# Kernel tuning notes

Measured on AMD Instinct MI355X. Metric: run time of the kernel, lower is better.

Reference implementation:

```python
import jax, jax.numpy as jnp
import numpy as np

HEAD_NUM = 16

def setup_inputs() -> dict:
    key = jax.random.key(0)
    k1, k2, k3, k4, k5 = jax.random.split(key, 5)
    B, S, F = 4, 2048, 1024
    return {
        "X": jax.random.normal(k1, (B, S, F), dtype=jnp.float32),
        "residual_score": jax.random.normal(k2, (B, S, F), dtype=jnp.float32),
        "wq": jax.random.normal(k3, (F, F), dtype=jnp.float32) * 0.05,
        "wk": jax.random.normal(k4, (F, F), dtype=jnp.float32) * 0.05,
        "wv": jax.random.normal(k5, (F, F), dtype=jnp.float32) * 0.05,
    }

def reference(X, residual_score, wq, wk, wv):
    B, S, F = X.shape
    H = HEAD_NUM
    D = F // H  # head dim
    # Original scales logits by sqrt(seq_len / head_num), not sqrt(head_dim).
    scale = jnp.sqrt(jnp.asarray(S / H, dtype=X.dtype))
    # QKV projections: [B,S,F] @ [F,F] -> [B,S,F], then split features into heads -> [B,H,S,D]
    def proj(w):
        y = jnp.einsum('bsf,fg->bsg', X, w)
        return y.reshape(B, S, H, D).transpose(0, 2, 1, 3)
    q, k, v = proj(wq), proj(wk), proj(wv)
    logits = jnp.einsum('bhsd,bhtd->bhst', q, k) / scale  # [B,H,S,S]
    attn = jax.nn.softmax(logits, axis=-1)
    effect = jnp.einsum('bhst,bhtd->bhsd', attn, v)  # [B,H,S,D]
    all_effects = effect.transpose(0, 2, 1, 3).reshape(B, S, F)
    out = all_effects + residual_score
    return (out, out)
```

## Files before the change

### kernel.cpp

```cpp
#include <hip/hip_runtime.h>
#include <hip/hip_bf16.h>
#include <stdint.h>

#define B_ 4
#define S_ 2048
#define F_ 1024
#define H_ 16
#define D_ 64
#define M_ (B_*S_)
#define OUTHALF ((size_t)B_*S_*F_)
#define KVB 64
#define QBLK 256

typedef __attribute__((ext_vector_type(4))) float f32x4;
typedef __attribute__((ext_vector_type(8))) short bf16x8;

__device__ __forceinline__ short f2bf(float f) {
  __hip_bfloat16 h = __float2bfloat16(f);
  return *reinterpret_cast<short*>(&h);
}

__device__ __forceinline__ void gl2lds16(const short* g, short* l) {
  __builtin_amdgcn_global_load_lds(
      (const __attribute__((address_space(1))) uint32_t*)g,
      (__attribute__((address_space(3))) uint32_t*)l, 16, 0, 0);
}

#define VMCNT_BAR(N)                                            \
  do {                                                          \
    asm volatile("s_waitcnt vmcnt(" #N ")" ::: "memory");       \
    __builtin_amdgcn_s_barrier();                               \
    asm volatile("" ::: "memory");                              \
  } while (0)

__global__ __launch_bounds__(256) void prep(
    const float* __restrict__ X, short* __restrict__ Xb,
    const float* __restrict__ wq, const float* __restrict__ wk, const float* __restrict__ wv,
    short* __restrict__ tq, short* __restrict__ tk, short* __restrict__ tv) {
  __shared__ float tile[32][33];
  const int bid = blockIdx.x;
  const int tid = threadIdx.x;
  if (bid < (M_ * F_) / (256 * 8)) {
    int i = (bid * 256 + tid) * 8;
    f32x4 a = *(const f32x4*)(X + i);
    f32x4 b = *(const f32x4*)(X + i + 4);
    bf16x8 o;
    o[0]=f2bf(a[0]); o[1]=f2bf(a[1]); o[2]=f2bf(a[2]); o[3]=f2bf(a[3]);
    o[4]=f2bf(b[0]); o[5]=f2bf(b[1]); o[6]=f2bf(b[2]); o[7]=f2bf(b[3]);
    *(bf16x8*)(Xb + i) = o;
    return;
  }
  const int b2 = bid - (M_ * F_) / (256 * 8);
  const int z = b2 >> 10;
  const int rem = b2 & 1023;
  const int bx = rem & 31, by = rem >> 5;
  const float* W = z == 0 ? wq : (z == 1 ? wk : wv);
  short* T = z == 0 ? tq : (z == 1 ? tk : tv);
  const int tx = tid & 31, ty = tid >> 5;
  int x = bx * 32 + tx;
  int y0 = by * 32;
  #pragma unroll
  for (int j = ty; j < 32; j += 8) tile[j][tx] = W[(size_t)(y0 + j) * F_ + x];
  __syncthreads();
  int x2 = y0 + tx;
  int y2 = bx * 32;
  #pragma unroll
  for (int j = ty; j < 32; j += 8) T[(size_t)(y2 + j) * F_ + x2] = f2bf(tile[tx][j]);
}

__global__ __launch_bounds__(256) void gemm_qkv(
    const short* __restrict__ Xb,
    const short* __restrict__ Wtq, const short* __restrict__ Wtk, const short* __restrict__ Wtv,
    short* __restrict__ Qb, short* __restrict__ Kb, short* __restrict__ Vt) {
  __shared__ short SMEM[4][4096];
  const int z = blockIdx.z;
  const short* Wt = z == 0 ? Wtq : (z == 1 ? Wtk : Wtv);
  const int m0 = blockIdx.x * 128, n0 = blockIdx.y * 128;
  const int tid = threadIdx.x, wid = tid >> 6, lane = tid & 63;
  const int wm = wid >> 1, wn = wid & 1;
  const int l15 = lane & 15, l4 = lane >> 4;

  f32x4 acc[4][4];
  #pragma unroll
  for (int i = 0; i < 4; ++i)
    #pragma unroll
    for (int j = 0; j < 4; ++j) acc[i][j] = {0.f, 0.f, 0.f, 0.f};

  const int srow = wid * 32 + (lane >> 2);
  const int scol = ((lane & 3) ^ ((lane >> 3) & 3)) * 8;
  const int rchunk = ((l15 >> 1) & 3);

  auto stage = [&](int buf, int k0) {
    gl2lds16(Xb + (size_t)(m0 + srow) * F_ + k0 + scol,      &SMEM[buf][(wid * 32) * 32]);
    gl2lds16(Xb + (size_t)(m0 + srow + 16) * F_ + k0 + scol, &SMEM[buf][(wid * 32 + 16) * 32]);
    gl2lds16(Wt + (size_t)(n0 + srow) * F_ + k0 + scol,      &SMEM[2 + buf][(wid * 32) * 32]);
    gl2lds16(Wt + (size_t)(n0 + srow + 16) * F_ + k0 + scol, &SMEM[2 + buf][(wid * 32 + 16) * 32]);
  };

  stage(0, 0);
  const int NT = F_ / 32;
  for (int t = 0; t < NT; ++t) {
    const int buf = t & 1;
    if (t + 1 < NT) {
      stage(buf ^ 1, (t + 1) * 32);
      VMCNT_BAR(4);
    } else {
      VMCNT_BAR(0);
    }
    bf16x8 a[4], b[4];
    const int rc = (l4 ^ rchunk) * 8;
    #pragma unroll
    for (int mf = 0; mf < 4; ++mf)
      a[mf] = *(const bf16x8*)&SMEM[buf][(wm * 64 + mf * 16 + l15) * 32 + rc];
    #pragma unroll
    for (int nf = 0; nf < 4; ++nf)
      b[nf] = *(const bf16x8*)&SMEM[2 + buf][(wn * 64 + nf * 16 + l15) * 32 + rc];
    __builtin_amdgcn_s_setprio(1);
    #pragma unroll
    for (int mf = 0; mf < 4; ++mf)
      #pragma unroll
      for (int nf = 0; nf < 4; ++nf)
        acc[mf][nf] = __builtin_amdgcn_mfma_f32_16x16x32_bf16(a[mf], b[nf], acc[mf][nf], 0, 0, 0);
    __builtin_amdgcn_s_setprio(0);
    __builtin_amdgcn_s_barrier();
    asm volatile("" ::: "memory");
  }

  const float qscale = 0.12751784477559752f;

  if (z == 2) {
    #pragma unroll
    for (int mf = 0; mf < 4; ++mf)
      #pragma unroll
      for (int nf = 0; nf < 4; ++nf)
        #pragma unroll
        for (int r = 0; r < 4; ++r) {
          float v = acc[mf][nf][r];
          int row = m0 + wm * 64 + mf * 16 + l4 * 4 + r;
          int col = n0 + wn * 64 + nf * 16 + l15;
          int bb = row >> 11, s = row & 2047, h = col >> 6, d = col & 63;
          int s5 = s & 31;
          int sp = (s & ~31) | (((s5 >> 2) & 3) << 3) | (((s5 >> 4) & 1) << 2) | (s5 & 3);
          Vt[((size_t)(bb * H_ + h) * D_ + d) * S_ + sp] = f2bf(v);
        }
  } else {
    short* Ep = &SMEM[0][0];
    short* dstBase = (z == 0) ? Qb : Kb;
    const float qs = (z == 0) ? qscale : 1.f;
    #pragma unroll
    for (int p = 0; p < 2; ++p) {
      __syncthreads();
      if (wm == p) {
        #pragma unroll
        for (int mf = 0; mf < 4; ++mf)
          #pragma unroll
          for (int nf = 0; nf < 4; ++nf)
            #pragma unroll
            for (int r = 0; r < 4; ++r)
              Ep[(mf * 16 + l4 * 4 + r) * 136 + wn * 64 + nf * 16 + l15] =
                  f2bf(acc[mf][nf][r] * qs);
      }
      __syncthreads();
      const int rr = tid >> 2, qt = tid & 3;
      const int grow = m0 + p * 64 + rr;
      const int gcol = n0 + qt * 32;
      const int bb = grow >> 11, s = grow & 2047;
      const int h = gcol >> 6, d0 = gcol & 63;
      short* dst = dstBase + (((size_t)(bb * H_ + h) * S_ + s) * D_ + d0);
      #pragma unroll
      for (int k = 0; k < 4; ++k)
        *(bf16x8*)(dst + k * 8) = *(const bf16x8*)&Ep[rr * 136 + qt * 32 + k * 8];
    }
  }
}

__global__ __launch_bounds__(512, 4) void attn_kernel(
    const short* __restrict__ Qb, const short* __restrict__ Kb, const short* __restrict__ Vt,
    const float* __restrict__ resid, float* __restrict__ out) {
  __shared__ short Ks[2][KVB][64];
  __shared__ short Vs[2][D_][KVB];
  const int bh = blockIdx.x;
  const int b = bh >> 4, h = bh & 15;
  const int qbase = blockIdx.y * QBLK;
  const int wid = threadIdx.x >> 6, lane = threadIdx.x & 63;
  const int l15 = lane & 15, l4 = lane >> 4;
  const short* Qp = Qb + (size_t)bh * S_ * D_;
  const short* Kp = Kb + (size_t)bh * S_ * D_;
  const short* Vp = Vt + (size_t)bh * D_ * S_;

  bf16x8 bq[2][2];
  #pragma unroll
  for (int g = 0; g < 2; ++g) {
    int qr = qbase + wid * 32 + g * 16 + l15;
    bq[g][0] = *(const bf16x8*)&Qp[qr * D_ + l4 * 8];
    bq[g][1] = *(const bf16x8*)&Qp[qr * D_ + 32 + l4 * 8];
  }

  bf16x8 aOnes;
  {
    short onebf = (short)0x3F80;
    #pragma unroll
    for (int i = 0; i < 8; ++i) aOnes[i] = (l15 == 0) ? onebf : (short)0;
  }

  const int sr = wid * 8 + (lane >> 3);
  const int ssrc = ((lane & 7) ^ (lane >> 3)) * 8;

  f32x4 acc[2][4];
  f32x4 accl[2];
  #pragma unroll
  for (int g = 0; g < 2; ++g) {
    accl[g] = {0.f, 0.f, 0.f, 0.f};
    #pragma unroll
    for (int df = 0; df < 4; ++df) acc[g][df] = {0.f, 0.f, 0.f, 0.f};
  }

  gl2lds16(Kp + (0 + sr) * D_ + ssrc, &Ks[0][wid * 8][0]);
  gl2lds16(Vp + (size_t)sr * S_ + 0 + ssrc, &Vs[0][wid * 8][0]);

  const int NT = S_ / KVB;
  for (int t = 0; t < NT; ++t) {
    const int buf = t & 1;
    __syncthreads();
    if (t + 1 < NT) {
      const int kv1 = (t + 1) * KVB;
      gl2lds16(Kp + (kv1 + sr) * D_ + ssrc, &Ks[buf ^ 1][wid * 8][0]);
      gl2lds16(Vp + (size_t)sr * S_ + kv1 + ssrc, &Vs[buf ^ 1][wid * 8][0]);
    }

    f32x4 sf[2][4];
    #pragma unroll
    for (int g = 0; g < 2; ++g)
      #pragma unroll
      for (int nf = 0; nf < 4; ++nf) sf[g][nf] = {0.f, 0.f, 0.f, 0.f};
    __builtin_amdgcn_s_setprio(1);
    #pragma unroll
    for (int nf = 0; nf < 4; ++nf) {
      int row = nf * 16 + l15;
      int c0 = (l4 ^ (row & 7)) * 8;
      int c1 = ((4 + l4) ^ (row & 7)) * 8;
      bf16x8 ak0 = *(const bf16x8*)&Ks[buf][row][c0];
      bf16x8 ak1 = *(const bf16x8*)&Ks[buf][row][c1];
      #pragma unroll
      for (int g = 0; g < 2; ++g) {
        sf[g][nf] = __builtin_amdgcn_mfma_f32_16x16x32_bf16(ak0, bq[g][0], sf[g][nf], 0, 0, 0);
        sf[g][nf] = __builtin_amdgcn_mfma_f32_16x16x32_bf16(ak1, bq[g][1], sf[g][nf], 0, 0, 0);
      }
    }
    __builtin_amdgcn_s_setprio(0);

    __builtin_amdgcn_s_setprio(1);
    #pragma unroll
    for (int bb = 0; bb < 2; ++bb) {
      bf16x8 p0, p1;
      #pragma unroll
      for (int r = 0; r < 4; ++r) {
        p0[r]     = f2bf(__builtin_amdgcn_exp2f(sf[0][2 * bb][r]));
        p0[4 + r] = f2bf(__builtin_amdgcn_exp2f(sf[0][2 * bb + 1][r]));
        p1[r]     = f2bf(__builtin_amdgcn_exp2f(sf[1][2 * bb][r]));
        p1[4 + r] = f2bf(__builtin_amdgcn_exp2f(sf[1][2 * bb + 1][r]));
      }
      #pragma unroll
      for (int df = 0; df < 4; ++df) {
        int row = df * 16 + l15;
        bf16x8 av = *(const bf16x8*)&Vs[buf][row][((4 * bb + l4) ^ (row & 7)) * 8];
        acc[0][df] = __builtin_amdgcn_mfma_f32_16x16x32_bf16(av, p0, acc[0][df], 0, 0, 0);
        acc[1][df] = __builtin_amdgcn_mfma_f32_16x16x32_bf16(av, p1, acc[1][df], 0, 0, 0);
      }
      accl[0] = __builtin_amdgcn_mfma_f32_16x16x32_bf16(aOnes, p0, accl[0], 0, 0, 0);
      accl[1] = __builtin_amdgcn_mfma_f32_16x16x32_bf16(aOnes, p1, accl[1], 0, 0, 0);
    }
    __builtin_amdgcn_s_setprio(0);
  }

  #pragma unroll
  for (int g = 0; g < 2; ++g) {
    float lg = __shfl(accl[g][0], l15);
    float rl = 1.f / lg;
    int s = qbase + wid * 32 + g * 16 + l15;
    #pragma unroll
    for (int df = 0; df < 4; ++df) {
      size_t oi = ((size_t)b * S_ + s) * F_ + h * D_ + df * 16 + l4 * 4;
      f32x4 rv = *(const f32x4*)&resid[oi];
      f32x4 ov;
      #pragma unroll
      for (int r = 0; r < 4; ++r) ov[r] = acc[g][df][r] * rl + rv[r];
      *(f32x4*)&out[oi] = ov;
      *(f32x4*)&out[oi + OUTHALF] = ov;
    }
  }
}

extern "C" void kernel_launch(void* const* d_in, const int* in_sizes, int n_in,
                              void* d_out, int out_size, void* d_ws, size_t ws_size,
                              hipStream_t stream) {
  (void)in_sizes; (void)n_in; (void)out_size; (void)ws_size;
  const float* X     = (const float*)d_in[0];
  const float* resid = (const float*)d_in[1];
  const float* wq    = (const float*)d_in[2];
  const float* wk    = (const float*)d_in[3];
  const float* wv    = (const float*)d_in[4];
  float* out = (float*)d_out;
  char* ws = (char*)d_ws;
  short* Xb  = (short*)(ws);
  short* Wtq = (short*)(ws + (16u << 20));
  short* Wtk = (short*)(ws + (18u << 20));
  short* Wtv = (short*)(ws + (20u << 20));
  short* Qb  = (short*)(ws + (22u << 20));
  short* Kb  = (short*)(ws + (38u << 20));
  short* Vt  = (short*)(ws + (54u << 20));

  prep<<<dim3((M_ * F_) / (256 * 8) + 3 * 1024), 256, 0, stream>>>(
      X, Xb, wq, wk, wv, Wtq, Wtk, Wtv);
  gemm_qkv<<<dim3(M_ / 128, F_ / 128, 3), 256, 0, stream>>>(Xb, Wtq, Wtk, Wtv, Qb, Kb, Vt);
  attn_kernel<<<dim3(B_ * H_, S_ / QBLK), 512, 0, stream>>>(Qb, Kb, Vt, resid, out);
}
```

Baseline: 168.2 us.

## Double KV tile to 128 and interleave QK and PV per 32-key chunk

Raises the KV block to 128 keys, so there are half as many loop iterations and barriers. Each thread now issues two K and two V async loads per tile, and the V swizzle is widened to 16 chunks. Inside the loop, the full score tile is no longer computed before the exponentials. Each 32-key chunk now does its QK MFMAs, exp and PV MFMAs in turn, which lowers live score registers. The cost is double the LDS buffer size, which may reduce occupancy.

```diff
diff --git a/kernel.cpp b/kernel.cpp
--- a/kernel.cpp
+++ b/kernel.cpp
@@ -9,7 +9,7 @@
 #define D_ 64
 #define M_ (B_*S_)
 #define OUTHALF ((size_t)B_*S_*F_)
-#define KVB 64
+#define KVB 128
 #define QBLK 256
 
 typedef __attribute__((ext_vector_type(4))) float f32x4;
@@ -203,8 +203,10 @@
     for (int i = 0; i < 8; ++i) aOnes[i] = (l15 == 0) ? onebf : (short)0;
   }
 
-  const int sr = wid * 8 + (lane >> 3);
-  const int ssrc = ((lane & 7) ^ (lane >> 3)) * 8;
+  const int ksr = wid * 16 + (lane >> 3);
+  const int ksc = ((lane & 7) ^ (ksr & 7)) * 8;
+  const int vr = wid * 4 + (lane >> 4);
+  const int vsc = ((lane & 15) ^ (vr & 15)) * 8;
 
   f32x4 acc[2][4];
   f32x4 accl[2];
@@ -215,8 +217,10 @@
     for (int df = 0; df < 4; ++df) acc[g][df] = {0.f, 0.f, 0.f, 0.f};
   }
 
-  gl2lds16(Kp + (0 + sr) * D_ + ssrc, &Ks[0][wid * 8][0]);
-  gl2lds16(Vp + (size_t)sr * S_ + 0 + ssrc, &Vs[0][wid * 8][0]);
+  gl2lds16(Kp + (0 + ksr) * D_ + ksc,            &Ks[0][wid * 16][0]);
+  gl2lds16(Kp + (0 + ksr + 8) * D_ + ksc,        &Ks[0][wid * 16 + 8][0]);
+  gl2lds16(Vp + (size_t)vr * S_ + 0 + vsc,       &Vs[0][wid * 4][0]);
+  gl2lds16(Vp + (size_t)(vr + 32) * S_ + 0 + vsc, &Vs[0][32 + wid * 4][0]);
 
   const int NT = S_ / KVB;
   for (int t = 0; t < NT; ++t) {
@@ -224,46 +228,44 @@
     __syncthreads();
     if (t + 1 < NT) {
       const int kv1 = (t + 1) * KVB;
-      gl2lds16(Kp + (kv1 + sr) * D_ + ssrc, &Ks[buf ^ 1][wid * 8][0]);
-      gl2lds16(Vp + (size_t)sr * S_ + kv1 + ssrc, &Vs[buf ^ 1][wid * 8][0]);
-    }
-
-    f32x4 sf[2][4];
-    #pragma unroll
-    for (int g = 0; g < 2; ++g)
-      #pragma unroll
-      for (int nf = 0; nf < 4; ++nf) sf[g][nf] = {0.f, 0.f, 0.f, 0.f};
+      gl2lds16(Kp + (kv1 + ksr) * D_ + ksc,             &Ks[buf ^ 1][wid * 16][0]);
+      gl2lds16(Kp + (kv1 + ksr + 8) * D_ + ksc,         &Ks[buf ^ 1][wid * 16 + 8][0]);
+      gl2lds16(Vp + (size_t)vr * S_ + kv1 + vsc,        &Vs[buf ^ 1][wid * 4][0]);
+      gl2lds16(Vp + (size_t)(vr + 32) * S_ + kv1 + vsc, &Vs[buf ^ 1][32 + wid * 4][0]);
+    }
+
     __builtin_amdgcn_s_setprio(1);
     #pragma unroll
-    for (int nf = 0; nf < 4; ++nf) {
-      int row = nf * 16 + l15;
-      int c0 = (l4 ^ (row & 7)) * 8;
-      int c1 = ((4 + l4) ^ (row & 7)) * 8;
-      bf16x8 ak0 = *(const bf16x8*)&Ks[buf][row][c0];
-      bf16x8 ak1 = *(const bf16x8*)&Ks[buf][row][c1];
-      #pragma unroll
-      for (int g = 0; g < 2; ++g) {
-        sf[g][nf] = __builtin_amdgcn_mfma_f32_16x16x32_bf16(ak0, bq[g][0], sf[g][nf], 0, 0, 0);
-        sf[g][nf] = __builtin_amdgcn_mfma_f32_16x16x32_bf16(ak1, bq[g][1], sf[g][nf], 0, 0, 0);
-      }
-    }
-    __builtin_amdgcn_s_setprio(0);
-
-    __builtin_amdgcn_s_setprio(1);
-    #pragma unroll
-    for (int bb = 0; bb < 2; ++bb) {
+    for (int bb = 0; bb < 4; ++bb) {
+      const int row0 = (2 * bb) * 16 + l15;
+      const int row1 = (2 * bb + 1) * 16 + l15;
+      bf16x8 ak00 = *(const bf16x8*)&Ks[buf][row0][(l4 ^ (row0 & 7)) * 8];
+      bf16x8 ak01 = *(const bf16x8*)&Ks[buf][row0][((4 + l4) ^ (row0 & 7)) * 8];
+      bf16x8 ak10 = *(const bf16x8*)&Ks[buf][row1][(l4 ^ (row1 & 7)) * 8];
+      bf16x8 ak11 = *(const bf16x8*)&Ks[buf][row1][((4 + l4) ^ (row1 & 7)) * 8];
+      f32x4 s00 = {0.f,0.f,0.f,0.f}, s01 = {0.f,0.f,0.f,0.f};
+      f32x4 s10 = {0.f,0.f,0.f,0.f}, s11 = {0.f,0.f,0.f,0.f};
+      s00 = __builtin_amdgcn_mfma_f32_16x16x32_bf16(ak00, bq[0][0], s00, 0, 0, 0);
+      s10 = __builtin_amdgcn_mfma_f32_16x16x32_bf16(ak00, bq[1][0], s10, 0, 0, 0);
+      s01 = __builtin_amdgcn_mfma_f32_16x16x32_bf16(ak10, bq[0][0], s01, 0, 0, 0);
+      s11 = __builtin_amdgcn_mfma_f32_16x16x32_bf16(ak10, bq[1][0], s11, 0, 0, 0);
+      s00 = __builtin_amdgcn_mfma_f32_16x16x32_bf16(ak01, bq[0][1], s00, 0, 0, 0);
+      s10 = __builtin_amdgcn_mfma_f32_16x16x32_bf16(ak01, bq[1][1], s10, 0, 0, 0);
+      s01 = __builtin_amdgcn_mfma_f32_16x16x32_bf16(ak11, bq[0][1], s01, 0, 0, 0);
+      s11 = __builtin_amdgcn_mfma_f32_16x16x32_bf16(ak11, bq[1][1], s11, 0, 0, 0);
+
       bf16x8 p0, p1;
       #pragma unroll
       for (int r = 0; r < 4; ++r) {
-        p0[r]     = f2bf(__builtin_amdgcn_exp2f(sf[0][2 * bb][r]));
-        p0[4 + r] = f2bf(__builtin_amdgcn_exp2f(sf[0][2 * bb + 1][r]));
-        p1[r]     = f2bf(__builtin_amdgcn_exp2f(sf[1][2 * bb][r]));
-        p1[4 + r] = f2bf(__builtin_amdgcn_exp2f(sf[1][2 * bb + 1][r]));
+        p0[r]     = f2bf(__builtin_amdgcn_exp2f(s00[r]));
+        p0[4 + r] = f2bf(__builtin_amdgcn_exp2f(s01[r]));
+        p1[r]     = f2bf(__builtin_amdgcn_exp2f(s10[r]));
+        p1[4 + r] = f2bf(__builtin_amdgcn_exp2f(s11[r]));
       }
       #pragma unroll
       for (int df = 0; df < 4; ++df) {
         int row = df * 16 + l15;
-        bf16x8 av = *(const bf16x8*)&Vs[buf][row][((4 * bb + l4) ^ (row & 7)) * 8];
+        bf16x8 av = *(const bf16x8*)&Vs[buf][row][((4 * bb + l4) ^ (row & 15)) * 8];
         acc[0][df] = __builtin_amdgcn_mfma_f32_16x16x32_bf16(av, p0, acc[0][df], 0, 0, 0);
         acc[1][df] = __builtin_amdgcn_mfma_f32_16x16x32_bf16(av, p1, acc[1][df], 0, 0, 0);
       }
```

Result: no change. 167.5 us (-0.4%).

## Halve per-wave query rows and interleave QK and PV per half tile

Applied to the files above, without the earlier changes.

Each wave now handles 16 query rows instead of 32, and the query block shrinks to 128 rows, so the grid doubles and each block does half the work. The QK^T scores are computed per 32-key half tile and fed straight into exp and the PV MFMAs, rather than scoring the whole 64-key tile first. This cuts accumulator and score registers, which can raise occupancy and shorten dependency chains. In exchange, K/V tiles loaded into LDS are reused by half as many query rows, which doubles global K/V traffic and the LDS reads per MFMA.

```diff
diff --git a/kernel.cpp b/kernel.cpp
--- a/kernel.cpp
+++ b/kernel.cpp
@@ -10,7 +10,7 @@
 #define M_ (B_*S_)
 #define OUTHALF ((size_t)B_*S_*F_)
 #define KVB 64
-#define QBLK 256
+#define QBLK 128
 
 typedef __attribute__((ext_vector_type(4))) float f32x4;
 typedef __attribute__((ext_vector_type(8))) short bf16x8;
@@ -188,12 +188,11 @@
   const short* Kp = Kb + (size_t)bh * S_ * D_;
   const short* Vp = Vt + (size_t)bh * D_ * S_;
 
-  bf16x8 bq[2][2];
-  #pragma unroll
-  for (int g = 0; g < 2; ++g) {
-    int qr = qbase + wid * 32 + g * 16 + l15;
-    bq[g][0] = *(const bf16x8*)&Qp[qr * D_ + l4 * 8];
-    bq[g][1] = *(const bf16x8*)&Qp[qr * D_ + 32 + l4 * 8];
+  bf16x8 bq0, bq1;
+  {
+    int qr = qbase + wid * 16 + l15;
+    bq0 = *(const bf16x8*)&Qp[qr * D_ + l4 * 8];
+    bq1 = *(const bf16x8*)&Qp[qr * D_ + 32 + l4 * 8];
   }
 
   bf16x8 aOnes;
@@ -206,14 +205,11 @@
   const int sr = wid * 8 + (lane >> 3);
   const int ssrc = ((lane & 7) ^ (lane >> 3)) * 8;
 
-  f32x4 acc[2][4];
-  f32x4 accl[2];
-  #pragma unroll
-  for (int g = 0; g < 2; ++g) {
-    accl[g] = {0.f, 0.f, 0.f, 0.f};
-    #pragma unroll
-    for (int df = 0; df < 4; ++df) acc[g][df] = {0.f, 0.f, 0.f, 0.f};
-  }
+  f32x4 acc[4];
+  f32x4 accl;
+  accl = {0.f, 0.f, 0.f, 0.f};
+  #pragma unroll
+  for (int df = 0; df < 4; ++df) acc[df] = {0.f, 0.f, 0.f, 0.f};
 
   gl2lds16(Kp + (0 + sr) * D_ + ssrc, &Ks[0][wid * 8][0]);
   gl2lds16(Vp + (size_t)sr * S_ + 0 + ssrc, &Vs[0][wid * 8][0]);
@@ -228,63 +224,49 @@
       gl2lds16(Vp + (size_t)sr * S_ + kv1 + ssrc, &Vs[buf ^ 1][wid * 8][0]);
     }
 
-    f32x4 sf[2][4];
-    #pragma unroll
-    for (int g = 0; g < 2; ++g)
-      #pragma unroll
-      for (int nf = 0; nf < 4; ++nf) sf[g][nf] = {0.f, 0.f, 0.f, 0.f};
     __builtin_amdgcn_s_setprio(1);
     #pragma unroll
-    for (int nf = 0; nf < 4; ++nf) {
-      int row = nf * 16 + l15;
-      int c0 = (l4 ^ (row & 7)) * 8;
-      int c1 = ((4 + l4) ^ (row & 7)) * 8;
-      bf16x8 ak0 = *(const bf16x8*)&Ks[buf][row][c0];
-      bf16x8 ak1 = *(const bf16x8*)&Ks[buf][row][c1];
-      #pragma unroll
-      for (int g = 0; g < 2; ++g) {
-        sf[g][nf] = __builtin_amdgcn_mfma_f32_16x16x32_bf16(ak0, bq[g][0], sf[g][nf], 0, 0, 0);
-        sf[g][nf] = __builtin_amdgcn_mfma_f32_16x16x32_bf16(ak1, bq[g][1], sf[g][nf], 0, 0, 0);
-      }
-    }
-    __builtin_amdgcn_s_setprio(0);
-
-    __builtin_amdgcn_s_setprio(1);
-    #pragma unroll
     for (int bb = 0; bb < 2; ++bb) {
-      bf16x8 p0, p1;
+      const int row0 = (2 * bb) * 16 + l15;
+      const int row1 = (2 * bb + 1) * 16 + l15;
+      bf16x8 ak00 = *(const bf16x8*)&Ks[buf][row0][(l4 ^ (row0 & 7)) * 8];
+      bf16x8 ak01 = *(const bf16x8*)&Ks[buf][row0][((4 + l4) ^ (row0 & 7)) * 8];
+      bf16x8 ak10 = *(const bf16x8*)&Ks[buf][row1][(l4 ^ (row1 & 7)) * 8];
+      bf16x8 ak11 = *(const bf16x8*)&Ks[buf][row1][((4 + l4) ^ (row1 & 7)) * 8];
+      f32x4 s0 = {0.f,0.f,0.f,0.f}, s1 = {0.f,0.f,0.f,0.f};
+      s0 = __builtin_amdgcn_mfma_f32_16x16x32_bf16(ak00, bq0, s0, 0, 0, 0);
+      s1 = __builtin_amdgcn_mfma_f32_16x16x32_bf16(ak10, bq0, s1, 0, 0, 0);
+      s0 = __builtin_amdgcn_mfma_f32_16x16x32_bf16(ak01, bq1, s0, 0, 0, 0);
+      s1 = __builtin_amdgcn_mfma_f32_16x16x32_bf16(ak11, bq1, s1, 0, 0, 0);
+
+      bf16x8 p;
       #pragma unroll
       for (int r = 0; r < 4; ++r) {
-        p0[r]     = f2bf(__builtin_amdgcn_exp2f(sf[0][2 * bb][r]));
-        p0[4 + r] = f2bf(__builtin_amdgcn_exp2f(sf[0][2 * bb + 1][r]));
-        p1[r]     = f2bf(__builtin_amdgcn_exp2f(sf[1][2 * bb][r]));
-        p1[4 + r] = f2bf(__builtin_amdgcn_exp2f(sf[1][2 * bb + 1][r]));
+        p[r]     = f2bf(__builtin_amdgcn_exp2f(s0[r]));
+        p[4 + r] = f2bf(__builtin_amdgcn_exp2f(s1[r]));
       }
       #pragma unroll
       for (int df = 0; df < 4; ++df) {
         int row = df * 16 + l15;
         bf16x8 av = *(const bf16x8*)&Vs[buf][row][((4 * bb + l4) ^ (row & 7)) * 8];
-        acc[0][df] = __builtin_amdgcn_mfma_f32_16x16x32_bf16(av, p0, acc[0][df], 0, 0, 0);
-        acc[1][df] = __builtin_amdgcn_mfma_f32_16x16x32_bf16(av, p1, acc[1][df], 0, 0, 0);
+        acc[df] = __builtin_amdgcn_mfma_f32_16x16x32_bf16(av, p, acc[df], 0, 0, 0);
       }
-      accl[0] = __builtin_amdgcn_mfma_f32_16x16x32_bf16(aOnes, p0, accl[0], 0, 0, 0);
-      accl[1] = __builtin_amdgcn_mfma_f32_16x16x32_bf16(aOnes, p1, accl[1], 0, 0, 0);
+      accl = __builtin_amdgcn_mfma_f32_16x16x32_bf16(aOnes, p, accl, 0, 0, 0);
     }
     __builtin_amdgcn_s_setprio(0);
   }
 
-  #pragma unroll
-  for (int g = 0; g < 2; ++g) {
-    float lg = __shfl(accl[g][0], l15);
+  {
+    float lg = __shfl(accl[0], l15);
     float rl = 1.f / lg;
-    int s = qbase + wid * 32 + g * 16 + l15;
+    int s = qbase + wid * 16 + l15;
     #pragma unroll
     for (int df = 0; df < 4; ++df) {
       size_t oi = ((size_t)b * S_ + s) * F_ + h * D_ + df * 16 + l4 * 4;
       f32x4 rv = *(const f32x4*)&resid[oi];
       f32x4 ov;
       #pragma unroll
-      for (int r = 0; r < 4; ++r) ov[r] = acc[g][df][r] * rl + rv[r];
+      for (int r = 0; r < 4; ++r) ov[r] = acc[df][r] * rl + rv[r];
       *(f32x4*)&out[oi] = ov;
       *(f32x4*)&out[oi + OUTHALF] = ov;
     }
```

After: 179.2 us. 6.5% more time.
